# Kernel tuning notes

Hardware: AMD Instinct MI355X
Metric: run time of the kernel (lower is better)

Reference implementation:

```python
import jax, jax.numpy as jnp
import numpy as np

B, CIN, NH, W, L, K = 16, 64, 64, 32, 4, 5
EPS = 1e-5
FORGET_BIAS = 1.0


def conv(x, w, b=None):
    # x: [B,C,H,W], w: [O,I,k,k] -> SAME padding, stride 1 (NCHW)
    y = jax.lax.conv_general_dilated(x, w, (1, 1), 'SAME',
                                     dimension_numbers=('NCHW', 'OIHW', 'NCHW'))
    if b is not None:
        y = y + b[None, :, None, None]
    return y


def ln(x, g, b):
    # torch LayerNorm([C,W,W]): normalize each sample over (C,H,W)
    m = jnp.mean(x, axis=(1, 2, 3), keepdims=True)
    v = jnp.mean((x - m) ** 2, axis=(1, 2, 3), keepdims=True)
    return (x - m) * jax.lax.rsqrt(v + EPS) * g[None] + b[None]


def attn_channel(q, kv):
    # q: [B,C,W,H], kv: [B,L,C,W,H]
    b, c, w, h = q.shape
    qf = q.reshape(b, c, w * h)                 # [B,C,HW]
    kf = kv.reshape(b, -1, w * h)               # [B,L*C,HW]
    a = jax.nn.softmax(jnp.einsum('bcp,blp->bcl', qf, kf), axis=2)  # [B,C,L*C]
    out = jnp.einsum('bcl,blp->bcp', a, kf)     # [B,C,HW]
    return out.reshape(b, c, w, h)


def attn_spatial(q, kv):
    # q: [B,C,W,H], kv: [B,L,C,W,H]
    b, c, w, h = q.shape
    qf = q.reshape(b, c, w * h).transpose(0, 2, 1)          # [B,HW,C]
    kf = kv.transpose(0, 1, 3, 4, 2).reshape(b, -1, c)      # [B,L*HW,C]
    a = jax.nn.softmax(jnp.einsum('bpc,bqc->bpq', qf, kf), axis=2)  # [B,HW,L*HW]
    out = jnp.einsum('bpq,bqc->bpc', a, kf)                 # [B,HW,C]
    return out.reshape(b, w, h, c).transpose(0, 3, 1, 2)


def setup_inputs() -> dict:
    key = jax.random.key(0)
    ks = iter(jax.random.split(key, 64))
    rn = lambda shape, s=1.0: jax.random.normal(next(ks), shape, jnp.float32) * s
    ones = lambda shape: jnp.ones(shape, jnp.float32)
    zeros = lambda shape: jnp.zeros(shape, jnp.float32)
    s = 0.02
    d = {}
    d['x_t'] = rn((B, CIN, W, W))
    d['h_t'] = rn((B, NH, W, W))
    d['c_t'] = rn((B, NH, W, W))
    d['c_historys'] = rn((B, L, NH, W, W))
    d['m_t'] = rn((B, NH, W, W))
    d['w_x'] = rn((7 * NH, CIN, K, K), s); d['ln_x_g'] = ones((7 * NH, W, W)); d['ln_x_b'] = zeros((7 * NH, W, W))
    d['w_h'] = rn((4 * NH, NH, K, K), s);  d['ln_h_g'] = ones((4 * NH, W, W)); d['ln_h_b'] = zeros((4 * NH, W, W))
    d['w_m'] = rn((3 * NH, NH, K, K), s);  d['ln_m_g'] = ones((3 * NH, W, W)); d['ln_m_b'] = zeros((3 * NH, W, W))
    d['w_o'] = rn((NH, 2 * NH, K, K), s);  d['ln_o_g'] = ones((NH, W, W));     d['ln_o_b'] = zeros((NH, W, W))
    d['w_last'] = rn((NH, 2 * NH, 1, 1), s)
    d['s_norm_g'] = ones((NH, W, W)); d['s_norm_b'] = zeros((NH, W, W))
    d['c_norm_g'] = ones((NH, W, W)); d['c_norm_b'] = zeros((NH, W, W))
    d['ca_w1'] = rn((NH, NH, K, K), s); d['ca_b1'] = zeros((NH,))
    d['ca_ln_g'] = ones((NH, W, W));    d['ca_ln_b'] = zeros((NH, W, W))
    d['ca_w2'] = rn((NH, NH, 1, 1), s); d['ca_b2'] = zeros((NH,))
    d['sa_w1'] = rn((NH, NH, K, K), s)
    d['sa_ln_g'] = ones((NH, W, W));    d['sa_ln_b'] = zeros((NH, W, W))
    d['sa_w2'] = rn((NH, NH, 1, 1), s)
    d['attn_w'] = rn((NH, NH, 1, 1), s)
    return d


def reference(x_t, h_t, c_t, c_historys, m_t,
              w_x, ln_x_g, ln_x_b, w_h, ln_h_g, ln_h_b, w_m, ln_m_g, ln_m_b,
              w_o, ln_o_g, ln_o_b, w_last,
              s_norm_g, s_norm_b, c_norm_g, c_norm_b,
              ca_w1, ca_b1, ca_ln_g, ca_ln_b, ca_w2, ca_b2,
              sa_w1, sa_ln_g, sa_ln_b, sa_w2, attn_w):
    x_concat = ln(conv(x_t, w_x), ln_x_g, ln_x_b)
    h_concat = ln(conv(h_t, w_h), ln_h_g, ln_h_b)
    m_concat = ln(conv(m_t, w_m), ln_m_g, ln_m_b)
    (i_x, f_x, g_x, i_xp, f_xp, g_xp, o_x) = jnp.split(x_concat, 7, axis=1)
    (i_h, f_h, g_h, o_h) = jnp.split(h_concat, 4, axis=1)
    (i_m, f_m, g_m) = jnp.split(m_concat, 3, axis=1)

    i_t = jax.nn.sigmoid(i_x + i_h)
    f_t = jax.nn.sigmoid(f_x + f_h + FORGET_BIAS)
    g_t = jnp.tanh(g_x + g_h)

    # attn_sum_fussion(c_t, query=f_t, keys=c_historys, values=c_historys)
    sp = ln(c_t + attn_spatial(f_t, c_historys), s_norm_g, s_norm_b)
    ch = ln(c_t + attn_channel(f_t, c_historys), c_norm_g, c_norm_b)
    s_a = conv(jax.nn.relu(ln(conv(sp, sa_w1), sa_ln_g, sa_ln_b)), sa_w2)
    c_a = conv(jax.nn.relu(ln(conv(ch, ca_w1, ca_b1), ca_ln_g, ca_ln_b)), ca_w2, ca_b2)
    attn = conv(s_a + c_a, attn_w)
    c_new = attn + i_t * g_t

    i_tp = jax.nn.sigmoid(i_xp + i_m)
    f_tp = jax.nn.sigmoid(f_xp + f_m + FORGET_BIAS)
    g_tp = jnp.tanh(g_xp + g_m)
    m_new = f_tp * m_t + i_tp * g_tp

    mem = jnp.concatenate((c_new, m_new), axis=1)
    o_t = jax.nn.sigmoid(o_x + o_h + ln(conv(mem, w_o), ln_o_g, ln_o_b))
    h_new = o_t * jnp.tanh(conv(mem, w_last))
    return h_new, c_new, m_new
```

## Files before the change

kernel.cpp:

```cpp
#include <hip/hip_runtime.h>
#include <hip/hip_bf16.h>

#define N1 (1u << 20)

typedef __attribute__((ext_vector_type(8))) short s8v;
typedef __attribute__((ext_vector_type(4))) float f4v;

static __device__ __forceinline__ float sigm(float x){ return 1.f/(1.f + __expf(-x)); }
static __device__ __forceinline__ float tanh_(float x){ return 1.f - 2.f/(__expf(2.f*x) + 1.f); }

static __device__ __forceinline__ ushort f2b(float f){
  union { float f; uint u; } x; x.f = f;
  uint r = x.u + 0x7FFFu + ((x.u >> 16) & 1u);
  return (ushort)(r >> 16);
}

static __device__ __forceinline__ void red_atomic2(float s, float q, float* d, int b, int t){
  #pragma unroll
  for (int m = 32; m; m >>= 1){ s += __shfl_xor(s, m); q += __shfl_xor(q, m); }
  if ((t & 63) == 0){ atomicAdd(&d[b*2], s); atomicAdd(&d[b*2+1], q); }
}

__global__ void k_zero(float* __restrict__ p){ p[threadIdx.x] = 0.f; }

__global__ __launch_bounds__(256) void k_wprep3(
    const float* __restrict__ sA, ushort* __restrict__ dA, int CoA, int CiA, int nA,
    const float* __restrict__ sB, ushort* __restrict__ dB, int CoB, int CiB, int nB,
    const float* __restrict__ sC, ushort* __restrict__ dC, int CoC, int CiC, int nC)
{
  int idx = blockIdx.x*256 + threadIdx.x;
  const float* s; ushort* d; int Co, Ci;
  if (idx < nA){ s=sA; d=dA; Co=CoA; Ci=CiA; }
  else if ((idx -= nA) < nB){ s=sB; d=dB; Co=CoB; Ci=CiB; }
  else if ((idx -= nB) < nC){ s=sC; d=dC; Co=CoC; Ci=CiC; }
  else return;
  int ci = idx % Ci; int r = idx / Ci; int co = r % Co; int tap = r / Co;
  d[idx] = f2b(s[((size_t)(co*Ci + ci))*25 + tap]);
}

struct Seg {
  const float* in; const ushort* w; const float* bias;
  float* out; float* ostat; const float* istat;
  const float* g; const float* bb;
  int Cin, Cout; float invN;
};
struct Segs3 { Seg s[3]; int b1, b2; };

template<int MT>
__global__ __launch_bounds__(256, 2) void k_convX(Segs3 Sg)
{
  constexpr int CO  = MT*16;
  constexpr int NW  = 5*CO*4;
  constexpr int ITW = (NW + 255) / 256;

  const int b = blockIdx.y;
  const int cog = blockIdx.x >> 2, pxblk = blockIdx.x & 3;
  const int si = (cog >= Sg.b1) + (cog >= Sg.b2);
  const Seg sg = Sg.s[si];
  const int base = si == 0 ? 0 : (si == 1 ? Sg.b1 : Sg.b2);
  const int co0 = (cog - base) * CO;
  const int r0 = pxblk << 3;
  const int t = threadIdx.x, w = t >> 6, l = t & 63;
  const int lane16 = l & 15, quad = l >> 4;

  __shared__ __align__(16) ushort S_[4][12][36][8];
  __shared__ __align__(16) ushort W_[2][4][5][CO][8];

  f4v acc[MT][4];
  #pragma unroll
  for (int mi = 0; mi < MT; ++mi)
    #pragma unroll
    for (int n = 0; n < 4; ++n) acc[mi][n] = (f4v){0.f,0.f,0.f,0.f};

  float mean = 0.f, rstd = 0.f;
  if (sg.istat){
    float s0 = sg.istat[b*2], s1 = sg.istat[b*2+1];
    mean = s0 * sg.invN;
    rstd = rsqrtf(s1 * sg.invN - mean*mean + 1e-5f);
  }

  const int ncc = sg.Cin >> 5;
  for (int cc = 0; cc < ncc; ++cc){
    __syncthreads();
    for (int idx = t; idx < 432; idx += 256){
      const int row = idx / 36, col = idx - row*36;
      const int ir = r0 - 2 + row, ic = col - 2;
      uint4 pk[4] = {make_uint4(0,0,0,0),make_uint4(0,0,0,0),make_uint4(0,0,0,0),make_uint4(0,0,0,0)};
      if ((unsigned)ir < 32u && (unsigned)ic < 32u){
        const int pix = (ir << 5) + ic;
        const float* bp = sg.in + (((size_t)(b*sg.Cin + (cc<<5))) << 10) + pix;
        #pragma unroll
        for (int q = 0; q < 4; ++q){
          uint hw[4];
          #pragma unroll
          for (int jj = 0; jj < 4; ++jj){
            const int c0 = q*8 + jj*2;
            float v0 = bp[(size_t)c0 << 10];
            float v1 = bp[(size_t)(c0+1) << 10];
            if (sg.g){
              const size_t li0 = (((size_t)((cc<<5)+c0)) << 10) + pix;
              v0 = (v0 - mean)*rstd*sg.g[li0] + sg.bb[li0];
              v1 = (v1 - mean)*rstd*sg.g[li0+1024] + sg.bb[li0+1024];
            }
            hw[jj] = (uint)f2b(v0) | ((uint)f2b(v1) << 16);
          }
          pk[q] = make_uint4(hw[0], hw[1], hw[2], hw[3]);
        }
      }
      #pragma unroll
      for (int q = 0; q < 4; ++q) *(uint4*)&S_[q][row][col][0] = pk[q];
    }
    #pragma unroll
    for (int it = 0; it < ITW; ++it){
      const int idx = t + it*256;
      if (ITW*256 == NW || idx < NW){
        const int q = idx & 3, r = idx >> 2;
        const int co = r & (CO - 1), dx = r / CO;
        uint4 wv = *(const uint4*)(sg.w + ((size_t)(dx*sg.Cout + co0+co))*sg.Cin + (cc<<5) + (q<<3));
        *(uint4*)&W_[0][q][dx][co][0] = wv;
      }
    }
    __syncthreads();
    for (int dy = 0; dy < 5; ++dy){
      uint4 wreg[ITW];
      if (dy < 4){
        #pragma unroll
        for (int it = 0; it < ITW; ++it){
          const int idx = t + it*256;
          if (ITW*256 == NW || idx < NW){
            const int q = idx & 3, r = idx >> 2;
            const int co = r & (CO - 1), dx = r / CO;
            wreg[it] = *(const uint4*)(sg.w + ((size_t)(((dy+1)*5+dx)*sg.Cout + co0+co))*sg.Cin + (cc<<5) + (q<<3));
          }
        }
      }
      #pragma unroll
      for (int dx = 0; dx < 5; ++dx){
        s8v a[MT];
        #pragma unroll
        for (int mi = 0; mi < MT; ++mi)
          a[mi] = *(const s8v*)&W_[dy & 1][quad][dx][mi*16 + lane16][0];
        #pragma unroll
        for (int n = 0; n < 4; ++n){
          const int srow = (w<<1) + (n>>1) + dy;
          const int col = ((n&1)<<4) + lane16 + dx;
          s8v bb = *(const s8v*)&S_[quad][srow][col][0];
          #pragma unroll
          for (int mi = 0; mi < MT; ++mi)
            acc[mi][n] = __builtin_amdgcn_mfma_f32_16x16x32_bf16(a[mi], bb, acc[mi][n], 0, 0, 0);
        }
      }
      if (dy < 4){
        #pragma unroll
        for (int it = 0; it < ITW; ++it){
          const int idx = t + it*256;
          if (ITW*256 == NW || idx < NW){
            const int q = idx & 3, r = idx >> 2;
            const int co = r & (CO - 1), dx = r / CO;
            *(uint4*)&W_[(dy+1) & 1][q][dx][co][0] = wreg[it];
          }
        }
      }
      __syncthreads();
    }
  }
  float lsum = 0.f, lsq = 0.f;
  #pragma unroll
  for (int mi = 0; mi < MT; ++mi){
    const int co = co0 + mi*16 + (quad<<2);
    #pragma unroll
    for (int n = 0; n < 4; ++n){
      const int row = r0 + (w<<1) + (n>>1);
      const int col = ((n&1)<<4) + lane16;
      #pragma unroll
      for (int i = 0; i < 4; ++i){
        float v = acc[mi][n][i] + (sg.bias ? sg.bias[co+i] : 0.f);
        sg.out[(((size_t)(b*sg.Cout + co + i)) << 10) + (row<<5) + col] = v;
        lsum += v; lsq += v*v;
      }
    }
  }
  if (sg.ostat) red_atomic2(lsum, lsq, sg.ostat, b, t);
}

__global__ __launch_bounds__(256) void k_prep(const float* __restrict__ src,
                                              ushort* __restrict__ outC,
                                              ushort* __restrict__ outT)
{
  const int plane = blockIdx.y;
  const int p0 = blockIdx.x << 6;
  const float* sp = src + ((size_t)plane << 16);
  __shared__ __align__(16) float T[64][68];
  const int t = threadIdx.x, c = t >> 2, g = t & 3;
  #pragma unroll
  for (int i = 0; i < 4; ++i){
    float4 f = *(const float4*)(sp + ((size_t)c << 10) + p0 + (g << 4) + (i << 2));
    *(float4*)&T[c][(g << 4) + (i << 2)] = f;
    if (outC){
      uint2 pk2;
      pk2.x = (uint)f2b(f.x) | ((uint)f2b(f.y) << 16);
      pk2.y = (uint)f2b(f.z) | ((uint)f2b(f.w) << 16);
      *(uint2*)(outC + ((((size_t)plane << 6) + c) << 10) + p0 + (g << 4) + (i << 2)) = pk2;
    }
  }
  __syncthreads();
  const int p = t >> 2, c0 = (t & 3) << 4;
  uint w4[8];
  #pragma unroll
  for (int k = 0; k < 8; ++k){
    ushort lo = f2b(T[c0 + 2*k][p]);
    ushort hi = f2b(T[c0 + 2*k + 1][p]);
    w4[k] = (uint)lo | ((uint)hi << 16);
  }
  ushort* dst = outT + ((((size_t)plane << 10) + p0 + p) << 6) + c0;
  *(uint4*)(dst)     = *(uint4*)&w4[0];
  *(uint4*)(dst + 8) = *(uint4*)&w4[4];
}

__global__ __launch_bounds__(256) void k_gates(
    const float* __restrict__ bufx, const float* __restrict__ bufh, const float* __restrict__ bufm,
    const float* __restrict__ lnxg, const float* __restrict__ lnxb,
    const float* __restrict__ lnhg, const float* __restrict__ lnhb,
    const float* __restrict__ lnmg, const float* __restrict__ lnmb,
    const float* __restrict__ m_t, const float* __restrict__ stats,
    float* __restrict__ ft, float* __restrict__ ig, float* __restrict__ osum,
    float* __restrict__ memo, float* __restrict__ out_m)
{
  const int idx = blockIdx.x*256 + threadIdx.x;
  const int b = idx >> 16, rem = idx & 65535;
  const int c = rem >> 10, p = rem & 1023;

  float mx = stats[b*2]      * (1.f/458752.f);
  float vx = stats[b*2+1]    * (1.f/458752.f) - mx*mx;  float rx = rsqrtf(vx + 1e-5f);
  float mh = stats[32+b*2]   * (1.f/262144.f);
  float vh = stats[32+b*2+1] * (1.f/262144.f) - mh*mh;  float rh = rsqrtf(vh + 1e-5f);
  float mm = stats[64+b*2]   * (1.f/196608.f);
  float vm = stats[64+b*2+1] * (1.f/196608.f) - mm*mm;  float rm = rsqrtf(vm + 1e-5f);

  auto LX = [&](int k){
    size_t ch = (size_t)k*64 + c; size_t gi = ((size_t)b*448 + ch)*1024 + p; size_t li = ch*1024 + p;
    return (bufx[gi] - mx)*rx*lnxg[li] + lnxb[li]; };
  auto LH = [&](int k){
    size_t ch = (size_t)k*64 + c; size_t gi = ((size_t)b*256 + ch)*1024 + p; size_t li = ch*1024 + p;
    return (bufh[gi] - mh)*rh*lnhg[li] + lnhb[li]; };
  auto LM = [&](int k){
    size_t ch = (size_t)k*64 + c; size_t gi = ((size_t)b*192 + ch)*1024 + p; size_t li = ch*1024 + p;
    return (bufm[gi] - mm)*rm*lnmg[li] + lnmb[li]; };

  float i_t = sigm(LX(0) + LH(0));
  float f_t = sigm(LX(1) + LH(1) + 1.f);
  float g_t = tanh_(LX(2) + LH(2));
  float i_p = sigm(LX(3) + LM(0));
  float f_p = sigm(LX(4) + LM(1) + 1.f);
  float g_p = tanh_(LX(5) + LM(2));
  float ox = LX(6), oh = LH(3);

  ft[idx]   = f_t;
  ig[idx]   = i_t * g_t;
  osum[idx] = ox + oh;
  float mn = f_p * m_t[idx] + i_p * g_p;
  out_m[idx] = mn;
  memo[((size_t)(b*128 + 64 + c) << 10) + p] = mn;
}

__global__ __launch_bounds__(256) void k_spat_mfma(
    const ushort* __restrict__ qT, const ushort* __restrict__ kvC, const ushort* __restrict__ kvT,
    const float* __restrict__ c_t, float* __restrict__ sp_raw, float* __restrict__ stats)
{
  const int p0 = blockIdx.x << 6, b = blockIdx.y;
  const int t = threadIdx.x, w = t >> 6, l = t & 63;
  const int lane16 = l & 15, quad = l >> 4;
  __shared__ __align__(16) ushort Kt[64][72];
  __shared__ __align__(16) ushort Kc[64][72];
  __shared__ __align__(16) ushort Eb[64][72];
  __shared__ __align__(16) float  XO[64][65];

  s8v qa0, qa1;
  {
    const ushort* qr = qT + ((((size_t)b << 10) + p0 + (w << 4) + lane16) << 6) + (quad << 3);
    qa0 = *(const s8v*)(qr);
    qa1 = *(const s8v*)(qr + 32);
  }
  f4v o0 = {0.f,0.f,0.f,0.f}, o1 = o0, o2 = o0, o3 = o0, dacc = o0;
  const short oneb = (short)0x3F80;
  const s8v ones = { oneb, oneb, oneb, oneb, oneb, oneb, oneb, oneb };

  const int r = t >> 2, g4 = (t & 3) << 4;
  for (int chunk = 0; chunk < 64; ++chunk){
    const int lidx = chunk >> 4, pk = (chunk & 15) << 6;
    __syncthreads();
    {
      const ushort* sc = kvC + ((((size_t)(b*4 + lidx) << 6) + r) << 10) + pk + g4;
      *(uint4*)&Kc[r][g4]     = *(const uint4*)(sc);
      *(uint4*)&Kc[r][g4 + 8] = *(const uint4*)(sc + 8);
      const ushort* st = kvT + ((((size_t)(b*4 + lidx) << 10) + pk + r) << 6) + g4;
      *(uint4*)&Kt[r][g4]     = *(const uint4*)(st);
      *(uint4*)&Kt[r][g4 + 8] = *(const uint4*)(st + 8);
    }
    __syncthreads();
    #pragma unroll
    for (int nt = 0; nt < 4; ++nt){
      const ushort* bt = &Kt[(nt << 4) + lane16][quad << 3];
      s8v b0 = *(const s8v*)(bt);
      s8v b1 = *(const s8v*)(bt + 32);
      f4v s = {0.f,0.f,0.f,0.f};
      s = __builtin_amdgcn_mfma_f32_16x16x32_bf16(qa0, b0, s, 0, 0, 0);
      s = __builtin_amdgcn_mfma_f32_16x16x32_bf16(qa1, b1, s, 0, 0, 0);
      #pragma unroll
      for (int i = 0; i < 4; ++i){
        float e = __expf(s[i] - 12.f);
        Eb[(w << 4) + (quad << 2) + i][(nt << 4) + lane16] = f2b(e);
      }
    }
    __syncthreads();
    #pragma unroll
    for (int ks = 0; ks < 2; ++ks){
      s8v ea = *(const s8v*)&Eb[(w << 4) + lane16][(ks << 5) + (quad << 3)];
      dacc = __builtin_amdgcn_mfma_f32_16x16x32_bf16(ea, ones, dacc, 0, 0, 0);
      s8v bc0 = *(const s8v*)&Kc[ 0 + lane16][(ks << 5) + (quad << 3)];
      s8v bc1 = *(const s8v*)&Kc[16 + lane16][(ks << 5) + (quad << 3)];
      s8v bc2 = *(const s8v*)&Kc[32 + lane16][(ks << 5) + (quad << 3)];
      s8v bc3 = *(const s8v*)&Kc[48 + lane16][(ks << 5) + (quad << 3)];
      o0 = __builtin_amdgcn_mfma_f32_16x16x32_bf16(ea, bc0, o0, 0, 0, 0);
      o1 = __builtin_amdgcn_mfma_f32_16x16x32_bf16(ea, bc1, o1, 0, 0, 0);
      o2 = __builtin_amdgcn_mfma_f32_16x16x32_bf16(ea, bc2, o2, 0, 0, 0);
      o3 = __builtin_amdgcn_mfma_f32_16x16x32_bf16(ea, bc3, o3, 0, 0, 0);
    }
  }
  {
    float inv0 = 1.f/dacc[0], inv1 = 1.f/dacc[1], inv2 = 1.f/dacc[2], inv3 = 1.f/dacc[3];
    const int pxl = (w << 4) + (quad << 2);
    XO[ 0 + lane16][pxl+0] = o0[0]*inv0; XO[ 0 + lane16][pxl+1] = o0[1]*inv1;
    XO[ 0 + lane16][pxl+2] = o0[2]*inv2; XO[ 0 + lane16][pxl+3] = o0[3]*inv3;
    XO[16 + lane16][pxl+0] = o1[0]*inv0; XO[16 + lane16][pxl+1] = o1[1]*inv1;
    XO[16 + lane16][pxl+2] = o1[2]*inv2; XO[16 + lane16][pxl+3] = o1[3]*inv3;
    XO[32 + lane16][pxl+0] = o2[0]*inv0; XO[32 + lane16][pxl+1] = o2[1]*inv1;
    XO[32 + lane16][pxl+2] = o2[2]*inv2; XO[32 + lane16][pxl+3] = o2[3]*inv3;
    XO[48 + lane16][pxl+0] = o3[0]*inv0; XO[48 + lane16][pxl+1] = o3[1]*inv1;
    XO[48 + lane16][pxl+2] = o3[2]*inv2; XO[48 + lane16][pxl+3] = o3[3]*inv3;
  }
  __syncthreads();
  {
    const int ch = t >> 2;
    float lsum = 0.f, lsq = 0.f;
    #pragma unroll
    for (int i = 0; i < 4; ++i){
      size_t gi = ((size_t)b << 16) + ((size_t)ch << 10) + p0 + g4 + (i << 2);
      float4 cv = *(const float4*)(c_t + gi);
      float4 ov;
      ov.x = cv.x + XO[ch][g4 + (i << 2) + 0];
      ov.y = cv.y + XO[ch][g4 + (i << 2) + 1];
      ov.z = cv.z + XO[ch][g4 + (i << 2) + 2];
      ov.w = cv.w + XO[ch][g4 + (i << 2) + 3];
      *(float4*)(sp_raw + gi) = ov;
      lsum += ov.x + ov.y + ov.z + ov.w;
      lsq  += ov.x*ov.x + ov.y*ov.y + ov.z*ov.z + ov.w*ov.w;
    }
    red_atomic2(lsum, lsq, stats, b, t);
  }
}

__global__ __launch_bounds__(256) void k_chlog_m(
    const ushort* __restrict__ ftC, const ushort* __restrict__ kvC, float* __restrict__ lg)
{
  const int lp = blockIdx.x, b = blockIdx.y;
  const int t = threadIdx.x, w = t >> 6, l = t & 63;
  const int lane16 = l & 15, quad = l >> 4;
  __shared__ __align__(16) ushort As[8][64][8];
  __shared__ __align__(16) ushort Bs[8][128][8];
  f4v acc[4][2];
  #pragma unroll
  for (int mi = 0; mi < 4; ++mi){ acc[mi][0] = (f4v){0.f,0.f,0.f,0.f}; acc[mi][1] = (f4v){0.f,0.f,0.f,0.f}; }

  for (int kc = 0; kc < 16; ++kc){
    __syncthreads();
    #pragma unroll
    for (int it = 0; it < 2; ++it){
      const int idx = t + it*256;
      const int c = idx >> 3, q = idx & 7;
      *(uint4*)&As[q][c][0] = *(const uint4*)(ftC + (((size_t)(b*64 + c)) << 10) + (kc<<6) + (q<<3));
    }
    #pragma unroll
    for (int it = 0; it < 4; ++it){
      const int idx = t + it*256;
      const int r2 = idx >> 3, q = idx & 7;
      const int plane = (b<<2) + (lp<<1) + (r2>>6);
      *(uint4*)&Bs[q][r2][0] = *(const uint4*)(kvC + ((((size_t)plane << 6) + (r2 & 63)) << 10) + (kc<<6) + (q<<3));
    }
    __syncthreads();
    #pragma unroll
    for (int ks = 0; ks < 2; ++ks){
      s8v a[4];
      #pragma unroll
      for (int mi = 0; mi < 4; ++mi)
        a[mi] = *(const s8v*)&As[(ks<<2)+quad][mi*16 + lane16][0];
      #pragma unroll
      for (int nt = 0; nt < 2; ++nt){
        s8v bb = *(const s8v*)&Bs[(ks<<2)+quad][(w<<5) + (nt<<4) + lane16][0];
        #pragma unroll
        for (int mi = 0; mi < 4; ++mi)
          acc[mi][nt] = __builtin_amdgcn_mfma_f32_16x16x32_bf16(a[mi], bb, acc[mi][nt], 0, 0, 0);
      }
    }
  }
  #pragma unroll
  for (int mi = 0; mi < 4; ++mi)
    #pragma unroll
    for (int nt = 0; nt < 2; ++nt)
      #pragma unroll
      for (int i = 0; i < 4; ++i){
        const int c = mi*16 + (quad<<2) + i;
        const int n = (lp<<7) + (w<<5) + (nt<<4) + lane16;
        lg[(((size_t)(b*64 + c)) << 8) + n] = acc[mi][nt][i];
      }
}

__global__ __launch_bounds__(256) void k_chsm(const float* __restrict__ a, ushort* __restrict__ ab)
{
  const int row  = blockIdx.x*4 + (threadIdx.x >> 6);
  const int lane = threadIdx.x & 63;
  const float* rp = a + ((size_t)row << 8);
  float v0 = rp[lane], v1 = rp[lane+64], v2 = rp[lane+128], v3 = rp[lane+192];
  float mx = fmaxf(fmaxf(v0, v1), fmaxf(v2, v3));
  #pragma unroll
  for (int m = 32; m; m >>= 1) mx = fmaxf(mx, __shfl_xor(mx, m));
  v0 = __expf(v0 - mx); v1 = __expf(v1 - mx); v2 = __expf(v2 - mx); v3 = __expf(v3 - mx);
  float s = v0 + v1 + v2 + v3;
  #pragma unroll
  for (int m = 32; m; m >>= 1) s += __shfl_xor(s, m);
  float inv = 1.f / s;
  ushort* op = ab + ((size_t)row << 8);
  op[lane] = f2b(v0*inv); op[lane+64] = f2b(v1*inv);
  op[lane+128] = f2b(v2*inv); op[lane+192] = f2b(v3*inv);
}

__global__ __launch_bounds__(256) void k_chout_m(
    const ushort* __restrict__ chlb, const ushort* __restrict__ kvT,
    const float* __restrict__ c_t, float* __restrict__ ch_raw, float* __restrict__ stats)
{
  const int p0 = blockIdx.x << 7, b = blockIdx.y;
  const int t = threadIdx.x, w = t >> 6, l = t & 63;
  const int lane16 = l & 15, quad = l >> 4;
  __shared__ __align__(16) ushort As[32][64][8];
  __shared__ __align__(16) ushort Bs[32][32][8];
  #pragma unroll
  for (int it = 0; it < 8; ++it){
    const int idx = t + it*256;
    const int c = idx >> 5, q = idx & 31;
    *(uint4*)&As[q][c][0] = *(const uint4*)(chlb + (((size_t)(b*64 + c)) << 8) + (q<<3));
  }
  __syncthreads();
  s8v a[8];
  #pragma unroll
  for (int ks = 0; ks < 8; ++ks)
    a[ks] = *(const s8v*)&As[(ks<<2)+quad][(w<<4) + lane16][0];
  float lsum = 0.f, lsq = 0.f;
  for (int pc = 0; pc < 4; ++pc){
    __syncthreads();
    #pragma unroll
    for (int it = 0; it < 4; ++it){
      const int idx = t + it*256;
      const int px = idx >> 5, q = idx & 31;
      const int plane = (b<<2) + (q>>3);
      *(uint4*)&Bs[q][px][0] = *(const uint4*)(kvT + ((((size_t)plane << 10) + p0 + (pc<<5) + px) << 6) + ((q&7)<<3));
    }
    __syncthreads();
    #pragma unroll
    for (int nt = 0; nt < 2; ++nt){
      f4v o = {0.f,0.f,0.f,0.f};
      #pragma unroll
      for (int ks = 0; ks < 8; ++ks){
        s8v bb = *(const s8v*)&Bs[(ks<<2)+quad][(nt<<4) + lane16][0];
        o = __builtin_amdgcn_mfma_f32_16x16x32_bf16(a[ks], bb, o, 0, 0, 0);
      }
      #pragma unroll
      for (int i = 0; i < 4; ++i){
        const int c = (w<<4) + (quad<<2) + i;
        const int px = p0 + (pc<<5) + (nt<<4) + lane16;
        size_t gi = ((size_t)b << 16) + ((size_t)c << 10) + px;
        float v = c_t[gi] + o[i];
        ch_raw[gi] = v;
        lsum += v; lsq += v*v;
      }
    }
  }
  red_atomic2(lsum, lsq, stats, b, t);
}

__global__ __launch_bounds__(256) void k_attnfinal(
    const float* __restrict__ samid, const float* __restrict__ camid,
    const float* __restrict__ stats_sa, const float* __restrict__ stats_ca,
    const float* __restrict__ salng, const float* __restrict__ salnb,
    const float* __restrict__ calng, const float* __restrict__ calnb,
    const float* __restrict__ wsa2, const float* __restrict__ wca2,
    const float* __restrict__ cab2, const float* __restrict__ wat,
    const float* __restrict__ ig, float* __restrict__ out_c, float* __restrict__ memo)
{
  const int p0 = blockIdx.x << 6, b = blockIdx.y, t = threadIdx.x;
  const int tc = t & 15, tp = t >> 4;
  __shared__ __align__(16) float R[64][68];
  __shared__ __align__(16) float Wl[64][68];
  __shared__ __align__(16) float Ms[64][68];
  const float invN = 1.f/65536.f;
  float acc[4][4] = {};
  #pragma unroll
  for (int pass = 0; pass < 2; ++pass){
    const float* mid = pass ? camid : samid;
    const float* st  = pass ? stats_ca : stats_sa;
    const float* g   = pass ? calng : salng;
    const float* bb  = pass ? calnb : salnb;
    const float* w   = pass ? wca2  : wsa2;
    float mean = st[b*2]*invN;
    float var  = st[b*2+1]*invN - mean*mean;
    float rstd = rsqrtf(var + 1e-5f);
    __syncthreads();
    {
      const int j = t & 63, c0 = t >> 6;
      for (int ci = c0; ci < 64; ci += 4){
        size_t gi = ((size_t)b << 16) + ((size_t)ci << 10) + p0 + j;
        size_t li = ((size_t)ci << 10) + p0 + j;
        float v = (mid[gi] - mean)*rstd*g[li] + bb[li];
        R[ci][j] = fmaxf(v, 0.f);
      }
      const int ci2 = t & 63, c20 = t >> 6;
      for (int c2 = c20; c2 < 64; c2 += 4) Wl[ci2][c2] = w[((size_t)c2 << 6) + ci2];
    }
    __syncthreads();
    for (int ci = 0; ci < 64; ++ci){
      float wv[4], rv[4];
      *(float4*)wv = *(const float4*)&Wl[ci][4*tc];
      *(float4*)rv = *(const float4*)&R[ci][4*tp];
      #pragma unroll
      for (int i = 0; i < 4; ++i)
        #pragma unroll
        for (int j = 0; j < 4; ++j)
          acc[i][j] = fmaf(wv[i], rv[j], acc[i][j]);
    }
  }
  {
    float b2[4];
    #pragma unroll
    for (int i = 0; i < 4; ++i) b2[i] = cab2[4*tc + i];
    #pragma unroll
    for (int i = 0; i < 4; ++i)
      #pragma unroll
      for (int j = 0; j < 4; ++j)
        Ms[4*tc+i][4*tp+j] = acc[i][j] + b2[i];
  }
  __syncthreads();
  {
    const int ci2 = t & 63, c20 = t >> 6;
    for (int c2 = c20; c2 < 64; c2 += 4) Wl[ci2][c2] = wat[((size_t)c2 << 6) + ci2];
  }
  __syncthreads();
  float acc2[4][4] = {};
  for (int c2 = 0; c2 < 64; ++c2){
    float wv[4], mv[4];
    *(float4*)wv = *(const float4*)&Wl[c2][4*tc];
    *(float4*)mv = *(const float4*)&Ms[c2][4*tp];
    #pragma unroll
    for (int i = 0; i < 4; ++i)
      #pragma unroll
      for (int j = 0; j < 4; ++j)
        acc2[i][j] = fmaf(wv[i], mv[j], acc2[i][j]);
  }
  #pragma unroll
  for (int i = 0; i < 4; ++i)
    #pragma unroll
    for (int j = 0; j < 4; ++j){
      size_t gi = ((size_t)b << 16) + ((size_t)(4*tc + i) << 10) + p0 + 4*tp + j;
      float v = acc2[i][j] + ig[gi];
      out_c[gi] = v;
      memo[((size_t)(b*128 + 4*tc + i) << 10) + p0 + 4*tp + j] = v;
    }
}

__global__ __launch_bounds__(256) void k_final(
    const float* __restrict__ memo, const float* __restrict__ wlast,
    const float* __restrict__ bufo, const float* __restrict__ osum,
    const float* __restrict__ stats_o, const float* __restrict__ lnog, const float* __restrict__ lnob,
    float* __restrict__ out_h)
{
  const int p0 = blockIdx.x << 6, b = blockIdx.y, t = threadIdx.x;
  const int tc = t & 15, tp = t >> 4;
  __shared__ __align__(16) float Msh[64][68];
  __shared__ __align__(16) float Wt[64][68];
  float acc[4][4] = {};
  #pragma unroll
  for (int half = 0; half < 2; ++half){
    __syncthreads();
    {
      const int j = t & 63, c0 = t >> 6;
      for (int ci = c0; ci < 64; ci += 4)
        Msh[ci][j] = memo[((size_t)(b*128 + half*64 + ci) << 10) + p0 + j];
      const int ci2 = t & 63, co0 = t >> 6;
      for (int co = co0; co < 64; co += 4) Wt[ci2][co] = wlast[((size_t)co << 7) + half*64 + ci2];
    }
    __syncthreads();
    for (int ci = 0; ci < 64; ++ci){
      float wv[4], mv[4];
      *(float4*)wv = *(const float4*)&Wt[ci][4*tc];
      *(float4*)mv = *(const float4*)&Msh[ci][4*tp];
      #pragma unroll
      for (int i = 0; i < 4; ++i)
        #pragma unroll
        for (int j = 0; j < 4; ++j)
          acc[i][j] = fmaf(wv[i], mv[j], acc[i][j]);
    }
  }
  float mean = stats_o[b*2]*(1.f/65536.f);
  float var  = stats_o[b*2+1]*(1.f/65536.f) - mean*mean;
  float rstd = rsqrtf(var + 1e-5f);
  #pragma unroll
  for (int i = 0; i < 4; ++i)
    #pragma unroll
    for (int j = 0; j < 4; ++j){
      const int co = 4*tc + i, p = p0 + 4*tp + j;
      size_t gi = ((size_t)b << 16) + ((size_t)co << 10) + p;
      size_t li = ((size_t)co << 10) + p;
      float lno = (bufo[gi] - mean)*rstd*lnog[li] + lnob[li];
      float o = sigm(osum[gi] + lno);
      out_h[gi] = o * tanh_(acc[i][j]);
    }
}

extern "C" void kernel_launch(void* const* d_in, const int* in_sizes, int n_in,
                              void* d_out, int out_size, void* d_ws, size_t ws_size,
                              hipStream_t stream)
{
  const float* x_t   = (const float*)d_in[0];
  const float* h_t   = (const float*)d_in[1];
  const float* c_t   = (const float*)d_in[2];
  const float* chist = (const float*)d_in[3];
  const float* m_t   = (const float*)d_in[4];
  const float* w_x   = (const float*)d_in[5];
  const float* lnxg  = (const float*)d_in[6];
  const float* lnxb  = (const float*)d_in[7];
  const float* w_h   = (const float*)d_in[8];
  const float* lnhg  = (const float*)d_in[9];
  const float* lnhb  = (const float*)d_in[10];
  const float* w_m   = (const float*)d_in[11];
  const float* lnmg  = (const float*)d_in[12];
  const float* lnmb  = (const float*)d_in[13];
  const float* w_o   = (const float*)d_in[14];
  const float* lnog  = (const float*)d_in[15];
  const float* lnob  = (const float*)d_in[16];
  const float* w_last= (const float*)d_in[17];
  const float* sng   = (const float*)d_in[18];
  const float* snb   = (const float*)d_in[19];
  const float* cng   = (const float*)d_in[20];
  const float* cnb   = (const float*)d_in[21];
  const float* ca_w1 = (const float*)d_in[22];
  const float* ca_b1 = (const float*)d_in[23];
  const float* calng = (const float*)d_in[24];
  const float* calnb = (const float*)d_in[25];
  const float* ca_w2 = (const float*)d_in[26];
  const float* ca_b2 = (const float*)d_in[27];
  const float* sa_w1 = (const float*)d_in[28];
  const float* salng = (const float*)d_in[29];
  const float* salnb = (const float*)d_in[30];
  const float* sa_w2 = (const float*)d_in[31];
  const float* attn_w= (const float*)d_in[32];

  float* out = (float*)d_out;
  float* ws  = (float*)d_ws;

  float* stats = ws;
  float* bufx  = ws + 1024;
  float* bufh  = bufx + 7*(size_t)N1;
  float* bufm  = bufh + 4*(size_t)N1;
  float* ft    = bufm + 3*(size_t)N1;
  float* ig    = ft   + (size_t)N1;
  float* osum  = ig   + (size_t)N1;
  float* memo  = osum + (size_t)N1;
  float* sp    = bufx;
  float* ch    = bufx + (size_t)N1;
  float* samid = bufx + 2*(size_t)N1;
  float* camid = bufx + 3*(size_t)N1;
  float* bufo  = bufx + 4*(size_t)N1;
  float* chl   = bufx + 5*(size_t)N1;
  ushort* kvC  = (ushort*)bufh;
  ushort* kvT  = kvC + 4*(size_t)N1;
  ushort* qT   = (ushort*)bufm;
  ushort* ftC  = qT + (size_t)N1;

  ushort* wbx = (ushort*)ft;
  ushort* wbh = wbx + 716800;
  ushort* wbm = wbh + 409600;
  ushort* wbo  = (ushort*)(chl + 262144);
  ushort* wbsa = wbo + 204800;
  ushort* wbca = wbsa + 102400;
  ushort* chlb = wbca + 102400;

  float* out_h = out;
  float* out_c = out + (size_t)N1;
  float* out_m = out + 2*(size_t)N1;

  k_zero<<<dim3(1), dim3(256), 0, stream>>>(stats);

  k_wprep3<<<dim3(5600), dim3(256), 0, stream>>>(
      w_x, wbx, 448, 64, 716800,
      w_h, wbh, 256, 64, 409600,
      w_m, wbm, 192, 64, 307200);

  {
    Segs3 XHM;
    XHM.s[0] = Seg{ x_t, wbx, nullptr, bufx, stats+0,  nullptr, nullptr, nullptr, 64, 448, 0.f };
    XHM.s[1] = Seg{ h_t, wbh, nullptr, bufh, stats+32, nullptr, nullptr, nullptr, 64, 256, 0.f };
    XHM.s[2] = Seg{ m_t, wbm, nullptr, bufm, stats+64, nullptr, nullptr, nullptr, 64, 192, 0.f };
    XHM.b1 = 7; XHM.b2 = 11;
    k_convX<4><<<dim3(56,16), dim3(256), 0, stream>>>(XHM);
  }

  k_gates<<<dim3(4096), dim3(256), 0, stream>>>(bufx, bufh, bufm, lnxg, lnxb, lnhg, lnhb,
                                                lnmg, lnmb, m_t, stats,
                                                ft, ig, osum, memo, out_m);

  k_wprep3<<<dim3(1600), dim3(256), 0, stream>>>(
      w_o,   wbo,  64, 128, 204800,
      sa_w1, wbsa, 64,  64, 102400,
      ca_w1, wbca, 64,  64, 102400);

  k_prep<<<dim3(16,64), dim3(256), 0, stream>>>(chist, kvC, kvT);
  k_prep<<<dim3(16,16), dim3(256), 0, stream>>>(ft, ftC, qT);

  k_spat_mfma<<<dim3(16,16), dim3(256), 0, stream>>>(qT, kvC, kvT, c_t, sp, stats+96);
  k_chlog_m<<<dim3(2,16), dim3(256), 0, stream>>>(ftC, kvC, chl);
  k_chsm  <<<dim3(256),  dim3(256), 0, stream>>>(chl, chlb);
  k_chout_m<<<dim3(8,16), dim3(256), 0, stream>>>(chlb, kvT, c_t, ch, stats+128);

  {
    Segs3 SC;
    SC.s[0] = Seg{ sp, wbsa, nullptr, samid, stats+160, stats+96,  sng, snb, 64, 64, 1.f/65536.f };
    SC.s[1] = Seg{ ch, wbca, ca_b1,   camid, stats+192, stats+128, cng, cnb, 64, 64, 1.f/65536.f };
    SC.s[2] = SC.s[1];
    SC.b1 = 2; SC.b2 = 1000;
    k_convX<2><<<dim3(16,16), dim3(256), 0, stream>>>(SC);
  }

  k_attnfinal<<<dim3(16,16), dim3(256), 0, stream>>>(samid, camid, stats+160, stats+192,
                                                     salng, salnb, calng, calnb,
                                                     sa_w2, ca_w2, ca_b2, attn_w,
                                                     ig, out_c, memo);

  {
    Segs3 O;
    O.s[0] = Seg{ memo, wbo, nullptr, bufo, stats+224, nullptr, nullptr, nullptr, 128, 64, 0.f };
    O.s[1] = O.s[0]; O.s[2] = O.s[0];
    O.b1 = 1000; O.b2 = 1000;
    k_convX<2><<<dim3(8,16), dim3(256), 0, stream>>>(O);
  }

  k_final<<<dim3(16,16), dim3(256), 0, stream>>>(memo, w_last, bufo, osum, stats+224,
                                                 lnog, lnob, out_h);
}
```

Before: 530.5 us.

## Pre-transpose conv inputs to channel-last bf16 and read weights directly from global

Adds transpose kernels that convert the conv inputs (x, h, m, the normalized sp/ch, and memo) into pixel-major bf16 with channels contiguous, folding the LayerNorm application into that prep pass. The conv kernel then loads its input tile with contiguous 16-byte vector loads instead of strided per-channel fp32 loads with bf16 conversion. Weights are re-laid out per 32-channel chunk in MFMA fragment order and read straight from global or L2, which removes the shared-memory weight double buffer and the per-dy barriers. Occupancy hints are raised. The cost is extra launches and extra workspace traffic, and the weight loads now go to global memory on every tap.

```diff
diff --git a/kernel.cpp b/kernel.cpp
--- a/kernel.cpp
+++ b/kernel.cpp
@@ -34,25 +34,95 @@
   else if ((idx -= nA) < nB){ s=sB; d=dB; Co=CoB; Ci=CiB; }
   else if ((idx -= nB) < nC){ s=sC; d=dC; Co=CoC; Ci=CiC; }
   else return;
-  int ci = idx % Ci; int r = idx / Ci; int co = r % Co; int tap = r / Co;
-  d[idx] = f2b(s[((size_t)(co*Ci + ci))*25 + tap]);
+  const int ci32 = idx & 31;
+  const int r  = idx >> 5;
+  const int co = r % Co;
+  const int r2 = r / Co;
+  const int tap = r2 % 25, cc = r2 / 25;
+  d[idx] = f2b(s[((size_t)(co*Ci + (cc<<5) + ci32))*25 + tap]);
+}
+
+struct PT { const float* s; ushort* d; const float* st; const float* g; const float* bb; };
+
+__global__ __launch_bounds__(256) void k_prepT3(PT ja, PT jb, PT jc, int n0, int n1, float invN)
+{
+  const int lp = blockIdx.y;
+  PT j; int pl;
+  if (lp < n0){ j = ja; pl = lp; }
+  else if (lp < n0 + n1){ j = jb; pl = lp - n0; }
+  else { j = jc; pl = lp - n0 - n1; }
+  const float* sp = j.s + ((size_t)pl << 16);
+  float mean = 0.f, rstd = 0.f;
+  if (j.st){
+    float s0 = j.st[pl*2], s1 = j.st[pl*2+1];
+    mean = s0*invN; rstd = rsqrtf(s1*invN - mean*mean + 1e-5f);
+  }
+  const int p0 = blockIdx.x << 6;
+  __shared__ __align__(16) float T[64][68];
+  const int t = threadIdx.x, c = t >> 2, g4 = t & 3;
+  #pragma unroll
+  for (int i = 0; i < 4; ++i){
+    const int px = (g4 << 4) + (i << 2);
+    float4 f = *(const float4*)(sp + ((size_t)c << 10) + p0 + px);
+    if (j.st){
+      const size_t li = ((size_t)c << 10) + p0 + px;
+      float4 gv = *(const float4*)(j.g + li);
+      float4 bv = *(const float4*)(j.bb + li);
+      f.x = (f.x - mean)*rstd*gv.x + bv.x;
+      f.y = (f.y - mean)*rstd*gv.y + bv.y;
+      f.z = (f.z - mean)*rstd*gv.z + bv.z;
+      f.w = (f.w - mean)*rstd*gv.w + bv.w;
+    }
+    *(float4*)&T[c][px] = f;
+  }
+  __syncthreads();
+  const int p = t >> 2, c0 = (t & 3) << 4;
+  uint w4[8];
+  #pragma unroll
+  for (int k = 0; k < 8; ++k){
+    ushort lo = f2b(T[c0 + 2*k][p]);
+    ushort hi = f2b(T[c0 + 2*k + 1][p]);
+    w4[k] = (uint)lo | ((uint)hi << 16);
+  }
+  ushort* dst = j.d + ((((size_t)pl << 10) + p0 + p) << 6) + c0;
+  *(uint4*)(dst)     = *(uint4*)&w4[0];
+  *(uint4*)(dst + 8) = *(uint4*)&w4[4];
+}
+
+__global__ __launch_bounds__(256) void k_prepTm(const float* __restrict__ src, ushort* __restrict__ dT)
+{
+  const int lp = blockIdx.y;
+  const int p0 = blockIdx.x << 6;
+  const float* sp = src + ((size_t)lp << 16);
+  __shared__ __align__(16) float T[64][68];
+  const int t = threadIdx.x, c = t >> 2, g4 = t & 3;
+  #pragma unroll
+  for (int i = 0; i < 4; ++i){
+    const int px = (g4 << 4) + (i << 2);
+    *(float4*)&T[c][px] = *(const float4*)(sp + ((size_t)c << 10) + p0 + px);
+  }
+  __syncthreads();
+  const int p = t >> 2, c0 = (t & 3) << 4;
+  uint w4[8];
+  #pragma unroll
+  for (int k = 0; k < 8; ++k)
+    w4[k] = (uint)f2b(T[c0 + 2*k][p]) | ((uint)f2b(T[c0 + 2*k + 1][p]) << 16);
+  ushort* dst = dT + ((((size_t)(lp >> 1) << 10) + p0 + p) << 7) + ((lp & 1) << 6) + c0;
+  *(uint4*)(dst)     = *(uint4*)&w4[0];
+  *(uint4*)(dst + 8) = *(uint4*)&w4[4];
 }
 
 struct Seg {
-  const float* in; const ushort* w; const float* bias;
-  float* out; float* ostat; const float* istat;
-  const float* g; const float* bb;
-  int Cin, Cout; float invN;
+  const ushort* inT; const ushort* w; const float* bias;
+  float* out; float* ostat;
+  int Cin, Cout;
 };
 struct Segs3 { Seg s[3]; int b1, b2; };
 
 template<int MT>
-__global__ __launch_bounds__(256, 2) void k_convX(Segs3 Sg)
-{
-  constexpr int CO  = MT*16;
-  constexpr int NW  = 5*CO*4;
-  constexpr int ITW = (NW + 255) / 256;
-
+__global__ __launch_bounds__(256, MT==4 ? 3 : 4) void k_convX(Segs3 Sg)
+{
+  constexpr int CO = MT*16;
   const int b = blockIdx.y;
   const int cog = blockIdx.x >> 2, pxblk = blockIdx.x & 3;
   const int si = (cog >= Sg.b1) + (cog >= Sg.b2);
@@ -62,22 +132,15 @@
   const int r0 = pxblk << 3;
   const int t = threadIdx.x, w = t >> 6, l = t & 63;
   const int lane16 = l & 15, quad = l >> 4;
+  const int lofs = (lane16 << 5) + (quad << 3);
 
   __shared__ __align__(16) ushort S_[4][12][36][8];
-  __shared__ __align__(16) ushort W_[2][4][5][CO][8];
 
   f4v acc[MT][4];
   #pragma unroll
   for (int mi = 0; mi < MT; ++mi)
     #pragma unroll
     for (int n = 0; n < 4; ++n) acc[mi][n] = (f4v){0.f,0.f,0.f,0.f};
-
-  float mean = 0.f, rstd = 0.f;
-  if (sg.istat){
-    float s0 = sg.istat[b*2], s1 = sg.istat[b*2+1];
-    mean = s0 * sg.invN;
-    rstd = rsqrtf(s1 * sg.invN - mean*mean + 1e-5f);
-  }
 
   const int ncc = sg.Cin >> 5;
   for (int cc = 0; cc < ncc; ++cc){
@@ -87,95 +150,47 @@
       const int ir = r0 - 2 + row, ic = col - 2;
       uint4 pk[4] = {make_uint4(0,0,0,0),make_uint4(0,0,0,0),make_uint4(0,0,0,0),make_uint4(0,0,0,0)};
       if ((unsigned)ir < 32u && (unsigned)ic < 32u){
-        const int pix = (ir << 5) + ic;
-        const float* bp = sg.in + (((size_t)(b*sg.Cin + (cc<<5))) << 10) + pix;
+        const ushort* bp = sg.inT + ((size_t)((b << 10) + (ir << 5) + ic)) * sg.Cin + (cc << 5);
         #pragma unroll
-        for (int q = 0; q < 4; ++q){
-          uint hw[4];
-          #pragma unroll
-          for (int jj = 0; jj < 4; ++jj){
-            const int c0 = q*8 + jj*2;
-            float v0 = bp[(size_t)c0 << 10];
-            float v1 = bp[(size_t)(c0+1) << 10];
-            if (sg.g){
-              const size_t li0 = (((size_t)((cc<<5)+c0)) << 10) + pix;
-              v0 = (v0 - mean)*rstd*sg.g[li0] + sg.bb[li0];
-              v1 = (v1 - mean)*rstd*sg.g[li0+1024] + sg.bb[li0+1024];
-            }
-            hw[jj] = (uint)f2b(v0) | ((uint)f2b(v1) << 16);
-          }
-          pk[q] = make_uint4(hw[0], hw[1], hw[2], hw[3]);
-        }
+        for (int q = 0; q < 4; ++q) pk[q] = *(const uint4*)(bp + (q << 3));
       }
       #pragma unroll
       for (int q = 0; q < 4; ++q) *(uint4*)&S_[q][row][col][0] = pk[q];
     }
-    #pragma unroll
-    for (int it = 0; it < ITW; ++it){
-      const int idx = t + it*256;
-      if (ITW*256 == NW || idx < NW){
-        const int q = idx & 3, r = idx >> 2;
-        const int co = r & (CO - 1), dx = r / CO;
-        uint4 wv = *(const uint4*)(sg.w + ((size_t)(dx*sg.Cout + co0+co))*sg.Cin + (cc<<5) + (q<<3));
-        *(uint4*)&W_[0][q][dx][co][0] = wv;
-      }
-    }
-    __syncthreads();
+    __syncthreads();
+    #pragma unroll
     for (int dy = 0; dy < 5; ++dy){
-      uint4 wreg[ITW];
-      if (dy < 4){
-        #pragma unroll
-        for (int it = 0; it < ITW; ++it){
-          const int idx = t + it*256;
-          if (ITW*256 == NW || idx < NW){
-            const int q = idx & 3, r = idx >> 2;
-            const int co = r & (CO - 1), dx = r / CO;
-            wreg[it] = *(const uint4*)(sg.w + ((size_t)(((dy+1)*5+dx)*sg.Cout + co0+co))*sg.Cin + (cc<<5) + (q<<3));
-          }
-        }
-      }
       #pragma unroll
       for (int dx = 0; dx < 5; ++dx){
+        const ushort* wp = sg.w + (((size_t)((cc*25 + dy*5 + dx)*sg.Cout + co0)) << 5) + lofs;
         s8v a[MT];
         #pragma unroll
         for (int mi = 0; mi < MT; ++mi)
-          a[mi] = *(const s8v*)&W_[dy & 1][quad][dx][mi*16 + lane16][0];
+          a[mi] = *(const s8v*)(wp + mi*512);
         #pragma unroll
         for (int n = 0; n < 4; ++n){
-          const int srow = (w<<1) + (n>>1) + dy;
-          const int col = ((n&1)<<4) + lane16 + dx;
+          const int srow = (w << 1) + (n >> 1) + dy;
+          const int col = ((n & 1) << 4) + lane16 + dx;
           s8v bb = *(const s8v*)&S_[quad][srow][col][0];
           #pragma unroll
           for (int mi = 0; mi < MT; ++mi)
             acc[mi][n] = __builtin_amdgcn_mfma_f32_16x16x32_bf16(a[mi], bb, acc[mi][n], 0, 0, 0);
         }
       }
-      if (dy < 4){
-        #pragma unroll
-        for (int it = 0; it < ITW; ++it){
-          const int idx = t + it*256;
-          if (ITW*256 == NW || idx < NW){
-            const int q = idx & 3, r = idx >> 2;
-            const int co = r & (CO - 1), dx = r / CO;
-            *(uint4*)&W_[(dy+1) & 1][q][dx][co][0] = wreg[it];
-          }
-        }
-      }
-      __syncthreads();
     }
   }
   float lsum = 0.f, lsq = 0.f;
   #pragma unroll
   for (int mi = 0; mi < MT; ++mi){
-    const int co = co0 + mi*16 + (quad<<2);
+    const int co = co0 + mi*16 + (quad << 2);
     #pragma unroll
     for (int n = 0; n < 4; ++n){
-      const int row = r0 + (w<<1) + (n>>1);
-      const int col = ((n&1)<<4) + lane16;
+      const int row = r0 + (w << 1) + (n >> 1);
+      const int col = ((n & 1) << 4) + lane16;
       #pragma unroll
       for (int i = 0; i < 4; ++i){
         float v = acc[mi][n][i] + (sg.bias ? sg.bias[co+i] : 0.f);
-        sg.out[(((size_t)(b*sg.Cout + co + i)) << 10) + (row<<5) + col] = v;
+        sg.out[(((size_t)(b*sg.Cout + co + i)) << 10) + (row << 5) + col] = v;
         lsum += v; lsq += v*v;
       }
     }
@@ -684,6 +699,13 @@
   ushort* qT   = (ushort*)bufm;
   ushort* ftC  = qT + (size_t)N1;
 
+  ushort* xT   = (ushort*)memo;
+  ushort* hT   = xT + (size_t)N1;
+  ushort* mT   = hT + (size_t)N1;
+  ushort* spT  = ftC + (size_t)N1;
+  ushort* chT  = spT + (size_t)N1;
+  ushort* memoT = (ushort*)bufx;
+
   ushort* wbx = (ushort*)ft;
   ushort* wbh = wbx + 716800;
   ushort* wbm = wbh + 409600;
@@ -704,10 +726,17 @@
       w_m, wbm, 192, 64, 307200);
 
   {
+    PT jx{ x_t, xT, nullptr, nullptr, nullptr };
+    PT jh{ h_t, hT, nullptr, nullptr, nullptr };
+    PT jm{ m_t, mT, nullptr, nullptr, nullptr };
+    k_prepT3<<<dim3(16,48), dim3(256), 0, stream>>>(jx, jh, jm, 16, 16, 0.f);
+  }
+
+  {
     Segs3 XHM;
-    XHM.s[0] = Seg{ x_t, wbx, nullptr, bufx, stats+0,  nullptr, nullptr, nullptr, 64, 448, 0.f };
-    XHM.s[1] = Seg{ h_t, wbh, nullptr, bufh, stats+32, nullptr, nullptr, nullptr, 64, 256, 0.f };
-    XHM.s[2] = Seg{ m_t, wbm, nullptr, bufm, stats+64, nullptr, nullptr, nullptr, 64, 192, 0.f };
+    XHM.s[0] = Seg{ xT, wbx, nullptr, bufx, stats+0,  64, 448 };
+    XHM.s[1] = Seg{ hT, wbh, nullptr, bufh, stats+32, 64, 256 };
+    XHM.s[2] = Seg{ mT, wbm, nullptr, bufm, stats+64, 64, 192 };
     XHM.b1 = 7; XHM.b2 = 11;
     k_convX<4><<<dim3(56,16), dim3(256), 0, stream>>>(XHM);
   }
@@ -730,9 +759,15 @@
   k_chout_m<<<dim3(8,16), dim3(256), 0, stream>>>(chlb, kvT, c_t, ch, stats+128);
 
   {
+    PT js{ sp, spT, stats+96,  sng, snb };
+    PT jc{ ch, chT, stats+128, cng, cnb };
+    k_prepT3<<<dim3(16,32), dim3(256), 0, stream>>>(js, jc, js, 16, 16, 1.f/65536.f);
+  }
+
+  {
     Segs3 SC;
-    SC.s[0] = Seg{ sp, wbsa, nullptr, samid, stats+160, stats+96,  sng, snb, 64, 64, 1.f/65536.f };
-    SC.s[1] = Seg{ ch, wbca, ca_b1,   camid, stats+192, stats+128, cng, cnb, 64, 64, 1.f/65536.f };
+    SC.s[0] = Seg{ spT, wbsa, nullptr, samid, stats+160, 64, 64 };
+    SC.s[1] = Seg{ chT, wbca, ca_b1,   camid, stats+192, 64, 64 };
     SC.s[2] = SC.s[1];
     SC.b1 = 2; SC.b2 = 1000;
     k_convX<2><<<dim3(16,16), dim3(256), 0, stream>>>(SC);
@@ -743,9 +778,11 @@
                                                      sa_w2, ca_w2, ca_b2, attn_w,
                                                      ig, out_c, memo);
 
+  k_prepTm<<<dim3(16,32), dim3(256), 0, stream>>>(memo, memoT);
+
   {
     Segs3 O;
-    O.s[0] = Seg{ memo, wbo, nullptr, bufo, stats+224, nullptr, nullptr, nullptr, 128, 64, 0.f };
+    O.s[0] = Seg{ memoT, wbo, nullptr, bufo, stats+224, 128, 64 };
     O.s[1] = O.s[0]; O.s[2] = O.s[0];
     O.b1 = 1000; O.b2 = 1000;
     k_convX<2><<<dim3(8,16), dim3(256), 0, stream>>>(O);
```

After: 550.6 us. +3.8%, slower.
